# Kernel optimization log

Hardware: AMD Instinct MI355X
Metric: run time of the kernel (lower is better)

## Reference

```python
import jax, jax.numpy as jnp
import numpy as np

N_HEADS = 8
N_HIDDEN = 32  # out_features // n_heads
NEG_SLOPE = 0.21
MASK_VAL = -1000000.0  # precision == '32'


def setup_inputs() -> dict:
    key = jax.random.key(0)
    k1, k2, k3, k4, k5 = jax.random.split(key, 5)
    B, N, Fin = 4, 512, 256
    HF = N_HEADS * N_HIDDEN
    h = jax.random.normal(k1, (B, N, Fin), dtype=jnp.float32)
    adj_mat = jax.random.randint(k2, (1, N, N, 1), 0, 2, dtype=jnp.int32)
    W_l = jax.random.normal(k3, (Fin, HF), dtype=jnp.float32) * 0.05
    W_r = jax.random.normal(k4, (Fin, HF), dtype=jnp.float32) * 0.05
    attn_w = jax.random.normal(k5, (N_HIDDEN,), dtype=jnp.float32) * 0.05
    return {"h": h, "adj_mat": adj_mat, "W_l": W_l, "W_r": W_r, "attn_w": attn_w}


def reference(h, adj_mat, W_l, W_r, attn_w):
    B, N, _ = h.shape
    H, F = N_HEADS, N_HIDDEN
    g_l = (h @ W_l).reshape(B, N, H, F)
    g_r = (h @ W_r).reshape(B, N, H, F)
    # torch repeat/repeat_interleave semantics: g_sum[b,i,j] = g_l[b,j] + g_r[b,i]
    g_sum = g_l[:, None, :, :, :] + g_r[:, :, None, :, :]  # (B, i, j, H, F)
    act = jnp.where(g_sum >= 0, g_sum, NEG_SLOPE * g_sum)
    e = jnp.einsum('bijhf,f->bijh', act, attn_w)  # (B, N, N, H)
    e = jnp.where(adj_mat == 0, MASK_VAL, e)
    a = jax.nn.softmax(e, axis=2)
    # dropout is identity in eval mode
    attn_res = jnp.einsum('bijh,bjhf->bihf', a, g_r)
    return attn_res.reshape(B, N, H * F)  # is_concat=True
```

## Files before the change

### kernel.cpp

```cpp
#include <hip/hip_runtime.h>
#include <math.h>

#define BB 4
#define NN 512
#define FIN 256
#define NH 8
#define FD 32
#define HF 256
#define CA 0.605f
#define CB 0.395f
#define IT 32
#define ESTR 268
#define GTS 260
#define GLX(j) ((j) ^ (((j) >> 5) & 7))
#define ALX(j) ((j) + ((j) >> 5))

typedef _Float16 h2_t __attribute__((ext_vector_type(2)));
union H2U { unsigned u; h2_t h; };
typedef __fp16 v8h __attribute__((ext_vector_type(8)));
typedef float v4f __attribute__((ext_vector_type(4)));
union U8 { uint4 u4; v8h h; };

__device__ __forceinline__ h2_t pkrtz(float a, float b) {
  auto r = __builtin_amdgcn_cvt_pkrtz(a, b);
  union { decltype(r) f; h2_t h; } u;
  u.f = r;
  return u.h;
}
__device__ __forceinline__ unsigned pkrtz_u(float a, float b) {
  H2U u; u.h = pkrtz(a, b);
  return u.u;
}

__device__ __forceinline__ float acc2(unsigned g, h2_t q, h2_t u, float acc) {
  H2U v; v.u = g;
  h2_t s = v.h + q;
  H2U a; a.h = s; a.u &= 0x7fff7fffu;
  return __builtin_amdgcn_fdot2(a.h, u, acc, false);
}

__device__ __forceinline__ float score16(uint4 g0, uint4 g1, uint4 g2, uint4 g3,
                                         const h2_t* qh, const h2_t* uh,
                                         float init) {
  float e0 = init, e1 = 0.f;
  e0 = acc2(g0.x, qh[0], uh[0], e0);
  e1 = acc2(g0.y, qh[1], uh[1], e1);
  e0 = acc2(g0.z, qh[2], uh[2], e0);
  e1 = acc2(g0.w, qh[3], uh[3], e1);
  e0 = acc2(g1.x, qh[4], uh[4], e0);
  e1 = acc2(g1.y, qh[5], uh[5], e1);
  e0 = acc2(g1.z, qh[6], uh[6], e0);
  e1 = acc2(g1.w, qh[7], uh[7], e1);
  e0 = acc2(g2.x, qh[8], uh[8], e0);
  e1 = acc2(g2.y, qh[9], uh[9], e1);
  e0 = acc2(g2.z, qh[10], uh[10], e0);
  e1 = acc2(g2.w, qh[11], uh[11], e1);
  e0 = acc2(g3.x, qh[12], uh[12], e0);
  e1 = acc2(g3.y, qh[13], uh[13], e1);
  e0 = acc2(g3.z, qh[14], uh[14], e0);
  e1 = acc2(g3.w, qh[15], uh[15], e1);
  return e0 + e1;
}

__global__ __launch_bounds__(256) void gemm_dual(
    const float* __restrict__ h, const float* __restrict__ Wl,
    const float* __restrict__ Wr, _Float16* __restrict__ glh,
    _Float16* __restrict__ grh) {
  const int t = threadIdx.x;
  const int row0 = blockIdx.x * 8;
  const float* __restrict__ W = blockIdx.y ? Wr : Wl;

  float acc[8] = {0.f, 0.f, 0.f, 0.f, 0.f, 0.f, 0.f, 0.f};
  const float* Wp = W + t;
  const float* hp = h + (size_t)row0 * FIN;

#pragma unroll 2
  for (int k4 = 0; k4 < FIN / 4; ++k4) {
    float4 hv[8];
#pragma unroll
    for (int r = 0; r < 8; ++r)
      hv[r] = *(const float4*)(hp + r * FIN + 4 * k4);
#pragma unroll
    for (int kk = 0; kk < 4; ++kk) {
      const float w = Wp[(size_t)(4 * k4 + kk) * HF];
#pragma unroll
      for (int r = 0; r < 8; ++r) {
        const float hval = (kk == 0) ? hv[r].x
                         : (kk == 1) ? hv[r].y
                         : (kk == 2) ? hv[r].z : hv[r].w;
        acc[r] = fmaf(hval, w, acc[r]);
      }
    }
  }

  _Float16* gp = (blockIdx.y ? grh : glh) + (size_t)row0 * HF + t;
#pragma unroll
  for (int r = 0; r < 8; ++r) gp[(size_t)r * HF] = (_Float16)acc[r];
}

__global__ __launch_bounds__(256, 2) void gat_attn(
    const _Float16* __restrict__ glh, const _Float16* __restrict__ grh,
    const int* __restrict__ adj, const float* __restrict__ aw,
    float* __restrict__ out) {
  __shared__ __align__(16) unsigned ubuf[32 * GTS];
  __shared__ __align__(16) unsigned e_s[IT][ESTR];
  __shared__ float Al_s[544];
  __shared__ float s_part[16][33];
  __shared__ float inv_l[IT];

  const int t = threadIdx.x;
  const int hh = blockIdx.x;
  const int i0 = blockIdx.y * IT;
  const int b = blockIdx.z;
  const int r0 = t & 15;
  const int jg = t >> 4;

  uint4* gl4 = (uint4*)ubuf;

  const _Float16* glp = glh + (size_t)b * NN * HF + hh * FD;

  h2_t wv[16], uh[16], qh[16], qh2[16];
  float a_r0 = 0.f, a_r1 = 0.f;
  {
#pragma unroll
    for (int f4 = 0; f4 < 8; ++f4) {
      const float4 w4 = *(const float4*)(aw + 4 * f4);
      wv[2 * f4] = pkrtz(CA * w4.x, CA * w4.y);
      wv[2 * f4 + 1] = pkrtz(CA * w4.z, CA * w4.w);
      uh[2 * f4] = pkrtz(CB * w4.x, CB * w4.y);
      uh[2 * f4 + 1] = pkrtz(CB * w4.z, CB * w4.w);
    }
    const uint4* qa =
        (const uint4*)(grh + (size_t)(b * NN + i0 + r0) * HF + hh * FD);
    const uint4* qb =
        (const uint4*)(grh + (size_t)(b * NN + i0 + r0 + 16) * HF + hh * FD);
    const uint4 q0 = qa[0], q1 = qa[1], q2 = qa[2], q3 = qa[3];
    const uint4 p0 = qb[0], p1 = qb[1], p2 = qb[2], p3 = qb[3];
    H2U z;
    z.u = q0.x; qh[0] = z.h;  z.u = q0.y; qh[1] = z.h;
    z.u = q0.z; qh[2] = z.h;  z.u = q0.w; qh[3] = z.h;
    z.u = q1.x; qh[4] = z.h;  z.u = q1.y; qh[5] = z.h;
    z.u = q1.z; qh[6] = z.h;  z.u = q1.w; qh[7] = z.h;
    z.u = q2.x; qh[8] = z.h;  z.u = q2.y; qh[9] = z.h;
    z.u = q2.z; qh[10] = z.h; z.u = q2.w; qh[11] = z.h;
    z.u = q3.x; qh[12] = z.h; z.u = q3.y; qh[13] = z.h;
    z.u = q3.z; qh[14] = z.h; z.u = q3.w; qh[15] = z.h;
    z.u = p0.x; qh2[0] = z.h;  z.u = p0.y; qh2[1] = z.h;
    z.u = p0.z; qh2[2] = z.h;  z.u = p0.w; qh2[3] = z.h;
    z.u = p1.x; qh2[4] = z.h;  z.u = p1.y; qh2[5] = z.h;
    z.u = p1.z; qh2[6] = z.h;  z.u = p1.w; qh2[7] = z.h;
    z.u = p2.x; qh2[8] = z.h;  z.u = p2.y; qh2[9] = z.h;
    z.u = p2.z; qh2[10] = z.h; z.u = p2.w; qh2[11] = z.h;
    z.u = p3.x; qh2[12] = z.h; z.u = p3.y; qh2[13] = z.h;
    z.u = p3.z; qh2[14] = z.h; z.u = p3.w; qh2[15] = z.h;
#pragma unroll
    for (int f2 = 0; f2 < 16; ++f2) {
      a_r0 = __builtin_amdgcn_fdot2(qh[f2], wv[f2], a_r0, false);
      a_r1 = __builtin_amdgcn_fdot2(qh2[f2], wv[f2], a_r1, false);
    }
  }

#pragma unroll
  for (int c = 0; c < 2; ++c) {
    const int j = t + 256 * c;
    const uint4* gp = (const uint4*)(glp + (size_t)j * HF);
    const uint4 g0 = gp[0], g1 = gp[1], g2 = gp[2], g3 = gp[3];
    const int jx = GLX(j);
    gl4[0 * NN + jx] = g0;
    gl4[1 * NN + jx] = g1;
    gl4[2 * NN + jx] = g2;
    gl4[3 * NN + jx] = g3;
    float s0 = 0.f, s1 = 0.f;
    H2U v;
#define ALD(gu, i)                                                  \
  v.u = gu.x; s0 = __builtin_amdgcn_fdot2(v.h, wv[i+0], s0, false); \
  v.u = gu.y; s1 = __builtin_amdgcn_fdot2(v.h, wv[i+1], s1, false); \
  v.u = gu.z; s0 = __builtin_amdgcn_fdot2(v.h, wv[i+2], s0, false); \
  v.u = gu.w; s1 = __builtin_amdgcn_fdot2(v.h, wv[i+3], s1, false);
    ALD(g0, 0) ALD(g1, 4) ALD(g2, 8) ALD(g3, 12)
#undef ALD
    Al_s[ALX(j)] = s0 + s1;
  }
  __syncthreads();

  {
    unsigned* erow0 = &e_s[r0][jg * 16];
    unsigned* erow1 = &e_s[r0 + 16][jg * 16];
    const int* adjp0 = adj + (size_t)(i0 + r0) * NN + jg * 32;
    const int* adjp1 = adj + (size_t)(i0 + r0 + 16) * NN + jg * 32;
    float srow0 = 0.f, srow1 = 0.f;
#pragma unroll 2
    for (int g4 = 0; g4 < 8; ++g4) {
      const int4 m0 = ((const int4*)adjp0)[g4];
      const int4 m1 = ((const int4*)adjp1)[g4];
      float p0[4], p1[4];
#pragma unroll
      for (int k = 0; k < 4; ++k) {
        const int j = jg * 32 + 4 * g4 + k;
        const int jx = GLX(j);
        const uint4 g0 = gl4[0 * NN + jx], g1 = gl4[1 * NN + jx];
        const uint4 g2 = gl4[2 * NN + jx], g3 = gl4[3 * NN + jx];
        const float al = Al_s[ALX(j)];
        const float e0 = score16(g0, g1, g2, g3, qh, uh, al + a_r0);
        const float e1 = score16(g0, g1, g2, g3, qh2, uh, al + a_r1);
        const int mk = (k == 0) ? m0.x : (k == 1) ? m0.y : (k == 2) ? m0.z : m0.w;
        const int nk = (k == 0) ? m1.x : (k == 1) ? m1.y : (k == 2) ? m1.z : m1.w;
        p0[k] = mk ? __expf(e0) : 0.f;
        p1[k] = nk ? __expf(e1) : 0.f;
      }
      srow0 += (p0[0] + p0[1]) + (p0[2] + p0[3]);
      srow1 += (p1[0] + p1[1]) + (p1[2] + p1[3]);
      uint2 w0, w1;
      w0.x = pkrtz_u(p0[0], p0[1]);
      w0.y = pkrtz_u(p0[2], p0[3]);
      w1.x = pkrtz_u(p1[0], p1[1]);
      w1.y = pkrtz_u(p1[2], p1[3]);
      *(uint2*)&erow0[2 * g4] = w0;
      *(uint2*)&erow1[2 * g4] = w1;
    }
    s_part[jg][r0] = srow0;
    s_part[jg][r0 + 16] = srow1;
  }
  __syncthreads();

  {
    const int fq = t & 7;
    const int jp0 = t >> 3;
    const unsigned* gbase =
        (const unsigned*)(grh + (size_t)b * NN * HF + hh * FD) + 2 * fq;
#pragma unroll
    for (int s2 = 0; s2 < 8; ++s2) {
      const int jp = jp0 + 32 * s2;
      const uint2 A = *(const uint2*)(gbase + (size_t)(2 * jp) * 128);
      const uint2 Bv = *(const uint2*)(gbase + (size_t)(2 * jp + 1) * 128);
      ubuf[(4 * fq + 0) * GTS + jp] = __builtin_amdgcn_perm(Bv.x, A.x, 0x05040100u);
      ubuf[(4 * fq + 1) * GTS + jp] = __builtin_amdgcn_perm(Bv.x, A.x, 0x07060302u);
      ubuf[(4 * fq + 2) * GTS + jp] = __builtin_amdgcn_perm(Bv.y, A.y, 0x05040100u);
      ubuf[(4 * fq + 3) * GTS + jp] = __builtin_amdgcn_perm(Bv.y, A.y, 0x07060302u);
    }
    if (t < IT) {
      float s = 0.f;
#pragma unroll
      for (int c = 0; c < 16; ++c) s += s_part[c][t];
      inv_l[t] = 1.f / s;
    }
  }
  __syncthreads();

  {
    const int lane = t & 63;
    const int wv3 = t >> 6;
    const int Mt = wv3 & 1, Nt = wv3 >> 1;
    const int l16 = lane & 15, q = lane >> 4;
    const unsigned* arow = &e_s[Mt * 16 + l16][0];
    const unsigned* brow = &ubuf[(Nt * 16 + l16) * GTS];
    v4f acc = {0.f, 0.f, 0.f, 0.f};
#pragma unroll
    for (int s = 0; s < 16; ++s) {
      U8 a; a.u4 = *(const uint4*)(arow + 16 * s + 4 * q);
      U8 bf; bf.u4 = *(const uint4*)(brow + 16 * s + 4 * q);
      acc = __builtin_amdgcn_mfma_f32_16x16x32_f16(a.h, bf.h, acc, 0, 0, 0);
    }
    float* op = out + (size_t)(b * NN + i0 + Mt * 16 + q * 4) * HF + hh * FD +
                Nt * 16 + l16;
#pragma unroll
    for (int r = 0; r < 4; ++r) {
      op[(size_t)r * HF] = acc[r] * inv_l[Mt * 16 + q * 4 + r];
    }
  }
}

extern "C" void kernel_launch(void* const* d_in, const int* in_sizes, int n_in,
                              void* d_out, int out_size, void* d_ws,
                              size_t ws_size, hipStream_t stream) {
  const float* h = (const float*)d_in[0];
  const int* adj = (const int*)d_in[1];
  const float* Wl = (const float*)d_in[2];
  const float* Wr = (const float*)d_in[3];
  const float* aw = (const float*)d_in[4];
  float* out = (float*)d_out;

  _Float16* glh = (_Float16*)d_ws;
  _Float16* grh = (_Float16*)((char*)d_ws + (size_t)BB * NN * HF * 2);

  dim3 gg(BB * NN / 8, 2, 1);
  gemm_dual<<<gg, 256, 0, stream>>>(h, Wl, Wr, glh, grh);

  dim3 ga(NH, NN / IT, BB);
  gat_attn<<<ga, 256, 0, stream>>>(glh, grh, adj, aw, out);
}
```

Measured before the change: 104.0 us.

## Double attention block threads to 512, one row per thread, split-K MFMA

Each attention block now has 512 threads instead of 256. Every thread scores one query row against 32 neighbours instead of two rows. The final MFMA reduction is split over two K halves, and the partial sums are combined through an extra shared-memory buffer and barrier. The aim is more parallelism per block and fewer registers per thread, which should hide latency better. The cost is an extra barrier, extra LDS traffic for the partial sums, and the g_l tile being reread per row instead of reused across two rows.

```diff
diff --git a/kernel.cpp b/kernel.cpp
--- a/kernel.cpp
+++ b/kernel.cpp
@@ -98,7 +98,7 @@
   for (int r = 0; r < 8; ++r) gp[(size_t)r * HF] = (_Float16)acc[r];
 }
 
-__global__ __launch_bounds__(256, 2) void gat_attn(
+__global__ __launch_bounds__(512, 4) void gat_attn(
     const _Float16* __restrict__ glh, const _Float16* __restrict__ grh,
     const int* __restrict__ adj, const float* __restrict__ aw,
     float* __restrict__ out) {
@@ -106,21 +106,22 @@
   __shared__ __align__(16) unsigned e_s[IT][ESTR];
   __shared__ float Al_s[544];
   __shared__ float s_part[16][33];
+  __shared__ float part3[32][33];
   __shared__ float inv_l[IT];
 
   const int t = threadIdx.x;
   const int hh = blockIdx.x;
   const int i0 = blockIdx.y * IT;
   const int b = blockIdx.z;
-  const int r0 = t & 15;
-  const int jg = t >> 4;
+  const int row = t & 31;
+  const int jg = t >> 5;
 
   uint4* gl4 = (uint4*)ubuf;
 
   const _Float16* glp = glh + (size_t)b * NN * HF + hh * FD;
 
-  h2_t wv[16], uh[16], qh[16], qh2[16];
-  float a_r0 = 0.f, a_r1 = 0.f;
+  h2_t wv[16], uh[16], qh[16];
+  float a_r = 0.f;
   {
 #pragma unroll
     for (int f4 = 0; f4 < 8; ++f4) {
@@ -131,11 +132,8 @@
       uh[2 * f4 + 1] = pkrtz(CB * w4.z, CB * w4.w);
     }
     const uint4* qa =
-        (const uint4*)(grh + (size_t)(b * NN + i0 + r0) * HF + hh * FD);
-    const uint4* qb =
-        (const uint4*)(grh + (size_t)(b * NN + i0 + r0 + 16) * HF + hh * FD);
+        (const uint4*)(grh + (size_t)(b * NN + i0 + row) * HF + hh * FD);
     const uint4 q0 = qa[0], q1 = qa[1], q2 = qa[2], q3 = qa[3];
-    const uint4 p0 = qb[0], p1 = qb[1], p2 = qb[2], p3 = qb[3];
     H2U z;
     z.u = q0.x; qh[0] = z.h;  z.u = q0.y; qh[1] = z.h;
     z.u = q0.z; qh[2] = z.h;  z.u = q0.w; qh[3] = z.h;
@@ -145,24 +143,13 @@
     z.u = q2.z; qh[10] = z.h; z.u = q2.w; qh[11] = z.h;
     z.u = q3.x; qh[12] = z.h; z.u = q3.y; qh[13] = z.h;
     z.u = q3.z; qh[14] = z.h; z.u = q3.w; qh[15] = z.h;
-    z.u = p0.x; qh2[0] = z.h;  z.u = p0.y; qh2[1] = z.h;
-    z.u = p0.z; qh2[2] = z.h;  z.u = p0.w; qh2[3] = z.h;
-    z.u = p1.x; qh2[4] = z.h;  z.u = p1.y; qh2[5] = z.h;
-    z.u = p1.z; qh2[6] = z.h;  z.u = p1.w; qh2[7] = z.h;
-    z.u = p2.x; qh2[8] = z.h;  z.u = p2.y; qh2[9] = z.h;
-    z.u = p2.z; qh2[10] = z.h; z.u = p2.w; qh2[11] = z.h;
-    z.u = p3.x; qh2[12] = z.h; z.u = p3.y; qh2[13] = z.h;
-    z.u = p3.z; qh2[14] = z.h; z.u = p3.w; qh2[15] = z.h;
-#pragma unroll
-    for (int f2 = 0; f2 < 16; ++f2) {
-      a_r0 = __builtin_amdgcn_fdot2(qh[f2], wv[f2], a_r0, false);
-      a_r1 = __builtin_amdgcn_fdot2(qh2[f2], wv[f2], a_r1, false);
-    }
-  }
-
-#pragma unroll
-  for (int c = 0; c < 2; ++c) {
-    const int j = t + 256 * c;
+#pragma unroll
+    for (int f2 = 0; f2 < 16; ++f2)
+      a_r = __builtin_amdgcn_fdot2(qh[f2], wv[f2], a_r, false);
+  }
+
+  {
+    const int j = t;
     const uint4* gp = (const uint4*)(glp + (size_t)j * HF);
     const uint4 g0 = gp[0], g1 = gp[1], g2 = gp[2], g3 = gp[3];
     const int jx = GLX(j);
@@ -184,42 +171,30 @@
   __syncthreads();
 
   {
-    unsigned* erow0 = &e_s[r0][jg * 16];
-    unsigned* erow1 = &e_s[r0 + 16][jg * 16];
-    const int* adjp0 = adj + (size_t)(i0 + r0) * NN + jg * 32;
-    const int* adjp1 = adj + (size_t)(i0 + r0 + 16) * NN + jg * 32;
-    float srow0 = 0.f, srow1 = 0.f;
+    unsigned* erow = &e_s[row][jg * 16];
+    const int* adjp = adj + (size_t)(i0 + row) * NN + jg * 32;
+    float srow = 0.f;
 #pragma unroll 2
     for (int g4 = 0; g4 < 8; ++g4) {
-      const int4 m0 = ((const int4*)adjp0)[g4];
-      const int4 m1 = ((const int4*)adjp1)[g4];
-      float p0[4], p1[4];
+      const int4 m = ((const int4*)adjp)[g4];
+      float p[4];
 #pragma unroll
       for (int k = 0; k < 4; ++k) {
         const int j = jg * 32 + 4 * g4 + k;
         const int jx = GLX(j);
-        const uint4 g0 = gl4[0 * NN + jx], g1 = gl4[1 * NN + jx];
-        const uint4 g2 = gl4[2 * NN + jx], g3 = gl4[3 * NN + jx];
-        const float al = Al_s[ALX(j)];
-        const float e0 = score16(g0, g1, g2, g3, qh, uh, al + a_r0);
-        const float e1 = score16(g0, g1, g2, g3, qh2, uh, al + a_r1);
-        const int mk = (k == 0) ? m0.x : (k == 1) ? m0.y : (k == 2) ? m0.z : m0.w;
-        const int nk = (k == 0) ? m1.x : (k == 1) ? m1.y : (k == 2) ? m1.z : m1.w;
-        p0[k] = mk ? __expf(e0) : 0.f;
-        p1[k] = nk ? __expf(e1) : 0.f;
+        const float e = score16(gl4[0 * NN + jx], gl4[1 * NN + jx],
+                                gl4[2 * NN + jx], gl4[3 * NN + jx], qh, uh,
+                                Al_s[ALX(j)] + a_r);
+        const int mk = (k == 0) ? m.x : (k == 1) ? m.y : (k == 2) ? m.z : m.w;
+        p[k] = mk ? __expf(e) : 0.f;
       }
-      srow0 += (p0[0] + p0[1]) + (p0[2] + p0[3]);
-      srow1 += (p1[0] + p1[1]) + (p1[2] + p1[3]);
-      uint2 w0, w1;
-      w0.x = pkrtz_u(p0[0], p0[1]);
-      w0.y = pkrtz_u(p0[2], p0[3]);
-      w1.x = pkrtz_u(p1[0], p1[1]);
-      w1.y = pkrtz_u(p1[2], p1[3]);
-      *(uint2*)&erow0[2 * g4] = w0;
-      *(uint2*)&erow1[2 * g4] = w1;
-    }
-    s_part[jg][r0] = srow0;
-    s_part[jg][r0 + 16] = srow1;
+      srow += (p[0] + p[1]) + (p[2] + p[3]);
+      uint2 w0;
+      w0.x = pkrtz_u(p[0], p[1]);
+      w0.y = pkrtz_u(p[2], p[3]);
+      *(uint2*)&erow[2 * g4] = w0;
+    }
+    s_part[jg][row] = srow;
   }
   __syncthreads();
 
@@ -229,8 +204,8 @@
     const unsigned* gbase =
         (const unsigned*)(grh + (size_t)b * NN * HF + hh * FD) + 2 * fq;
 #pragma unroll
-    for (int s2 = 0; s2 < 8; ++s2) {
-      const int jp = jp0 + 32 * s2;
+    for (int s2 = 0; s2 < 4; ++s2) {
+      const int jp = jp0 + 64 * s2;
       const uint2 A = *(const uint2*)(gbase + (size_t)(2 * jp) * 128);
       const uint2 Bv = *(const uint2*)(gbase + (size_t)(2 * jp + 1) * 128);
       ubuf[(4 * fq + 0) * GTS + jp] = __builtin_amdgcn_perm(Bv.x, A.x, 0x05040100u);
@@ -250,22 +225,31 @@
   {
     const int lane = t & 63;
     const int wv3 = t >> 6;
-    const int Mt = wv3 & 1, Nt = wv3 >> 1;
+    const int Mt = wv3 & 1, Nt = (wv3 >> 1) & 1, Kh = wv3 >> 2;
     const int l16 = lane & 15, q = lane >> 4;
     const unsigned* arow = &e_s[Mt * 16 + l16][0];
     const unsigned* brow = &ubuf[(Nt * 16 + l16) * GTS];
     v4f acc = {0.f, 0.f, 0.f, 0.f};
 #pragma unroll
-    for (int s = 0; s < 16; ++s) {
+    for (int s = 8 * Kh; s < 8 * Kh + 8; ++s) {
       U8 a; a.u4 = *(const uint4*)(arow + 16 * s + 4 * q);
       U8 bf; bf.u4 = *(const uint4*)(brow + 16 * s + 4 * q);
       acc = __builtin_amdgcn_mfma_f32_16x16x32_f16(a.h, bf.h, acc, 0, 0, 0);
     }
-    float* op = out + (size_t)(b * NN + i0 + Mt * 16 + q * 4) * HF + hh * FD +
-                Nt * 16 + l16;
-#pragma unroll
-    for (int r = 0; r < 4; ++r) {
-      op[(size_t)r * HF] = acc[r] * inv_l[Mt * 16 + q * 4 + r];
+    if (Kh) {
+#pragma unroll
+      for (int r = 0; r < 4; ++r)
+        part3[Mt * 16 + q * 4 + r][Nt * 16 + l16] = acc[r];
+    }
+    __syncthreads();
+    if (!Kh) {
+      float* op = out + (size_t)(b * NN + i0 + Mt * 16 + q * 4) * HF +
+                  hh * FD + Nt * 16 + l16;
+#pragma unroll
+      for (int r = 0; r < 4; ++r)
+        op[(size_t)r * HF] =
+            (acc[r] + part3[Mt * 16 + q * 4 + r][Nt * 16 + l16]) *
+            inv_l[Mt * 16 + q * 4 + r];
     }
   }
 }
@@ -287,5 +271,5 @@
   gemm_dual<<<gg, 256, 0, stream>>>(h, Wl, Wr, glh, grh);
 
   dim3 ga(NH, NN / IT, BB);
-  gat_attn<<<ga, 256, 0, stream>>>(glh, grh, adj, aw, out);
-}
+  gat_attn<<<ga, 512, 0, stream>>>(glh, grh, adj, aw, out);
+}
```

Result: no change. 104.6 us (+0.6%).
